# Optimization experiments

Measured on AMD Instinct MI355X. Metric: run time of the kernel, lower is better.

Reference implementation:

```python
import jax, jax.numpy as jnp
import numpy as np

N_NODES = 100000
N_EDGES = 1600000
N_GRAPHS = 256
D_IN = 128
D_HID = 128
D_OUT = 7
BN_EPS = 1e-5


def setup_inputs() -> dict:
    key = jax.random.key(0)
    ks = jax.random.split(key, 16)
    def lin(k, fan_in, fan_out):
        # torch.nn.Linear init: U(-1/sqrt(fan_in), 1/sqrt(fan_in)); stored as [in, out]
        bound = 1.0 / np.sqrt(fan_in)
        kw, kb = jax.random.split(k)
        w = jax.random.uniform(kw, (fan_in, fan_out), jnp.float32, -bound, bound)
        b = jax.random.uniform(kb, (fan_out,), jnp.float32, -bound, bound)
        return w, b
    x = jax.random.normal(ks[0], (N_NODES, D_IN), jnp.float32)
    edge_index = jax.random.randint(ks[1], (2, N_EDGES), 0, N_NODES, jnp.int64)
    batch = jnp.sort(jax.random.randint(ks[2], (N_NODES,), 0, N_GRAPHS, jnp.int64))
    w1a, b1a = lin(ks[3], D_IN, D_HID)
    w1b, b1b = lin(ks[4], D_HID, D_HID)
    w2a, b2a = lin(ks[5], D_HID, D_HID)
    w2b, b2b = lin(ks[6], D_HID, D_HID)
    wl, bl = lin(ks[7], D_HID, D_OUT)
    g1 = jnp.ones((D_HID,), jnp.float32); be1 = jnp.zeros((D_HID,), jnp.float32)
    g2 = jnp.ones((D_HID,), jnp.float32); be2 = jnp.zeros((D_HID,), jnp.float32)
    return {"x": x, "w1a": w1a, "b1a": b1a, "w1b": w1b, "b1b": b1b,
            "g1": g1, "be1": be1,
            "w2a": w2a, "b2a": b2a, "w2b": w2b, "b2b": b2b,
            "g2": g2, "be2": be2,
            "wl": wl, "bl": bl,
            "edge_index": edge_index, "batch": batch}


def gin_conv(x, edge_index, wa, ba, wb, bb):
    src, dst = edge_index[0], edge_index[1]
    # sum aggregation of source features at target nodes (eps = 0)
    agg = jax.ops.segment_sum(x[src], dst, num_segments=N_NODES)
    h = x + agg
    h = jnp.maximum(h @ wa + ba, 0.0)
    return h @ wb + bb


def batch_norm(x, gamma, beta):
    mean = jnp.mean(x, axis=0)
    var = jnp.mean(jnp.square(x - mean), axis=0)  # biased, training-mode stats
    return (x - mean) * (gamma / jnp.sqrt(var + BN_EPS)) + beta


def reference(x, w1a, b1a, w1b, b1b, g1, be1,
              w2a, b2a, w2b, b2b, g2, be2,
              wl, bl, edge_index, batch):
    h = gin_conv(x, edge_index, w1a, b1a, w1b, b1b)
    h = jnp.maximum(batch_norm(h, g1, be1), 0.0)
    h = gin_conv(h, edge_index, w2a, b2a, w2b, b2b)
    h = jnp.maximum(batch_norm(h, g2, be2), 0.0)
    # global mean pool over graphs
    sums = jax.ops.segment_sum(h, batch, num_segments=N_GRAPHS)
    cnts = jax.ops.segment_sum(jnp.ones((h.shape[0],), h.dtype), batch, num_segments=N_GRAPHS)
    pooled = sums / jnp.maximum(cnts, 1.0)[:, None]  # [G, D_HID]
    logits = pooled @ wl + bl
    return jax.nn.log_softmax(logits, axis=1)
```

## Files before the change

kernel.cpp:

```cpp
#include <hip/hip_runtime.h>
#include <math.h>

#define NN 100000
#define NE 1600000
#define NG 256
#define D 128
#define EPS 1e-5f
#define MAXDEG 64
#define NBINS 196
#define BINSZ 512
#define BINCAP 12288
#define GRID_BIN 250
#define EPB_A 6400
#define GRID_CAST 6250
#define GRID_TW 32
#define GRID_GEMM 782

typedef __attribute__((ext_vector_type(8))) short s16x8;
typedef __attribute__((ext_vector_type(4))) float f32x4;

__device__ __forceinline__ ushort f2b(float f) {
    uint u = __float_as_uint(f);
    uint r = (u + 0x7fffu + ((u >> 16) & 1u)) >> 16;
    return (ushort)r;
}
__device__ __forceinline__ float blo(uint u) { return __uint_as_float(u << 16); }
__device__ __forceinline__ float bhi(uint u) { return __uint_as_float(u & 0xFFFF0000u); }

#define SWZW(lin) ((lin) ^ ((((lin) >> 8) & 7) << 4))

__global__ __launch_bounds__(256) void prep1(const int* __restrict__ esrc, const int* __restrict__ edst,
                                             uint* __restrict__ binbuf, int* __restrict__ bincnt,
                                             const float* __restrict__ x, ushort* __restrict__ xb,
                                             const float* __restrict__ w1a, const float* __restrict__ w1b,
                                             const float* __restrict__ w2a, const float* __restrict__ w2b,
                                             ushort* __restrict__ Wt) {
    int b = blockIdx.x;
    if (b < GRID_BIN) {
        __shared__ int cnt[NBINS], lbase[NBINS];
        const int ebase = b * EPB_A;
        for (int it = 0; it < 7; ++it) {
            for (int t = threadIdx.x; t < NBINS; t += 256) cnt[t] = 0;
            __syncthreads();
            int e = ebase + it * 1024 + threadIdx.x * 4;
            bool valid = (e < ebase + EPB_A);
            int4 s = make_int4(0, 0, 0, 0), d = make_int4(0, 0, 0, 0);
            if (valid) {
                s = *(const int4*)(esrc + e);
                d = *(const int4*)(edst + e);
            }
            int b0 = d.x >> 9, b1 = d.y >> 9, b2 = d.z >> 9, b3 = d.w >> 9;
            int o0 = 0, o1 = 0, o2 = 0, o3 = 0;
            if (valid) {
                o0 = atomicAdd(&cnt[b0], 1);
                o1 = atomicAdd(&cnt[b1], 1);
                o2 = atomicAdd(&cnt[b2], 1);
                o3 = atomicAdd(&cnt[b3], 1);
            }
            __syncthreads();
            for (int t = threadIdx.x; t < NBINS; t += 256)
                lbase[t] = (cnt[t] > 0) ? atomicAdd(&bincnt[t], cnt[t]) : 0;
            __syncthreads();
            if (valid) {
                uint p0 = (uint)(lbase[b0] + o0), p1 = (uint)(lbase[b1] + o1);
                uint p2 = (uint)(lbase[b2] + o2), p3 = (uint)(lbase[b3] + o3);
                if (p0 < BINCAP) binbuf[b0 * BINCAP + p0] = ((uint)(d.x & 511) << 17) | (uint)s.x;
                if (p1 < BINCAP) binbuf[b1 * BINCAP + p1] = ((uint)(d.y & 511) << 17) | (uint)s.y;
                if (p2 < BINCAP) binbuf[b2 * BINCAP + p2] = ((uint)(d.z & 511) << 17) | (uint)s.z;
                if (p3 < BINCAP) binbuf[b3 * BINCAP + p3] = ((uint)(d.w & 511) << 17) | (uint)s.w;
            }
        }
    } else if (b < GRID_BIN + GRID_CAST) {
        int i = (b - GRID_BIN) * 256 + threadIdx.x;
        if (i * 8 < NN * D) {
            float4 v0 = *(const float4*)(x + i * 8);
            float4 v1 = *(const float4*)(x + i * 8 + 4);
            ushort o[8] = {f2b(v0.x), f2b(v0.y), f2b(v0.z), f2b(v0.w),
                           f2b(v1.x), f2b(v1.y), f2b(v1.z), f2b(v1.w)};
            *(uint4*)(xb + i * 8) = *(uint4*)o;
        }
    } else {
        int by = b - GRID_BIN - GRID_CAST;
        int wsel = by >> 3, bx = by & 7;
        const float* W = (wsel == 0) ? w1a : (wsel == 1) ? w1b : (wsel == 2) ? w2a : w2b;
        ushort* T = Wt + wsel * 16384;
        for (int i = bx * 256 + threadIdx.x; i < 16384; i += 8 * 256) {
            int k = i >> 7, cc = i & 127;
            T[(cc << 7) | k] = f2b(W[i]);
        }
    }
}

__global__ __launch_bounds__(256) void drain(const uint* __restrict__ binbuf, const int* __restrict__ bincnt,
                                             int* __restrict__ deg, int* __restrict__ slots) {
    const int bin = blockIdx.x;
    int n = bincnt[bin]; if (n > BINCAP) n = BINCAP;
    __shared__ int cur[BINSZ];
    cur[threadIdx.x] = 0;
    cur[threadIdx.x + 256] = 0;
    __syncthreads();
    const uint* bp = binbuf + bin * BINCAP;
    const int base = bin << 9;
    int i = threadIdx.x;
    for (; i + 768 < n; i += 1024) {
        uint u0 = bp[i], u1 = bp[i + 256], u2 = bp[i + 512], u3 = bp[i + 768];
        int l0 = u0 >> 17, l1 = u1 >> 17, l2 = u2 >> 17, l3 = u3 >> 17;
        int p0 = atomicAdd(&cur[l0], 1);
        int p1 = atomicAdd(&cur[l1], 1);
        int p2 = atomicAdd(&cur[l2], 1);
        int p3 = atomicAdd(&cur[l3], 1);
        slots[((base + l0) << 6) | (p0 & 63)] = (int)(u0 & 0x1FFFFu);
        slots[((base + l1) << 6) | (p1 & 63)] = (int)(u1 & 0x1FFFFu);
        slots[((base + l2) << 6) | (p2 & 63)] = (int)(u2 & 0x1FFFFu);
        slots[((base + l3) << 6) | (p3 & 63)] = (int)(u3 & 0x1FFFFu);
    }
    for (; i < n; i += 256) {
        uint u0 = bp[i];
        int l0 = u0 >> 17;
        int p0 = atomicAdd(&cur[l0], 1);
        slots[((base + l0) << 6) | (p0 & 63)] = (int)(u0 & 0x1FFFFu);
    }
    __syncthreads();
    int node = base + threadIdx.x;
    if (node < NN) deg[node] = cur[threadIdx.x];
    node += 256;
    if (node < NN) deg[node] = cur[threadIdx.x + 256];
}

template <int FUSE_BN>
__global__ __launch_bounds__(256) void gather_slots(ushort* __restrict__ out, const ushort* __restrict__ feat,
                                                    const int* __restrict__ deg, const int* __restrict__ slots,
                                                    const float* __restrict__ scale, const float* __restrict__ shift) {
    int node = __builtin_amdgcn_readfirstlane(blockIdx.x * 4 + (threadIdx.x >> 6));
    if (node >= NN) return;
    int lane = threadIdx.x & 63;
    int n = deg[node];
    n = (n > MAXDEG) ? MAXDEG : n;
    const int* sl = slots + (node << 6);
    float scx = 1.f, scy = 1.f, shx = 0.f, shy = 0.f;
    if (FUSE_BN) {
        float2 sc = *(const float2*)(scale + lane * 2);
        float2 sh = *(const float2*)(shift + lane * 2);
        scx = sc.x; scy = sc.y; shx = sh.x; shy = sh.y;
    }
    uint ub = *(const uint*)(feat + node * D + lane * 2);
    float axv[8], ayv[8];
#pragma unroll
    for (int j = 0; j < 8; ++j) { axv[j] = 0.f; ayv[j] = 0.f; }
    if (FUSE_BN) {
        axv[0] = fmaxf(fmaf(blo(ub), scx, shx), 0.f);
        ayv[0] = fmaxf(fmaf(bhi(ub), scy, shy), 0.f);
    } else {
        axv[0] = blo(ub); ayv[0] = bhi(ub);
    }
    int e = 0;
    for (; e + 15 < n; e += 16) {
        uint u[16];
#pragma unroll
        for (int j = 0; j < 16; ++j) u[j] = *(const uint*)(feat + sl[e + j] * D + lane * 2);
#pragma unroll
        for (int j = 0; j < 16; ++j) {
            int j8 = j & 7;
            if (FUSE_BN) {
                axv[j8] += fmaxf(fmaf(blo(u[j]), scx, shx), 0.f);
                ayv[j8] += fmaxf(fmaf(bhi(u[j]), scy, shy), 0.f);
            } else {
                axv[j8] += blo(u[j]); ayv[j8] += bhi(u[j]);
            }
        }
    }
    for (; e + 7 < n; e += 8) {
        uint u[8];
#pragma unroll
        for (int j = 0; j < 8; ++j) u[j] = *(const uint*)(feat + sl[e + j] * D + lane * 2);
#pragma unroll
        for (int j = 0; j < 8; ++j) {
            if (FUSE_BN) {
                axv[j] += fmaxf(fmaf(blo(u[j]), scx, shx), 0.f);
                ayv[j] += fmaxf(fmaf(bhi(u[j]), scy, shy), 0.f);
            } else {
                axv[j] += blo(u[j]); ayv[j] += bhi(u[j]);
            }
        }
    }
    for (; e + 3 < n; e += 4) {
        uint u[4];
#pragma unroll
        for (int j = 0; j < 4; ++j) u[j] = *(const uint*)(feat + sl[e + j] * D + lane * 2);
#pragma unroll
        for (int j = 0; j < 4; ++j) {
            if (FUSE_BN) {
                axv[j] += fmaxf(fmaf(blo(u[j]), scx, shx), 0.f);
                ayv[j] += fmaxf(fmaf(bhi(u[j]), scy, shy), 0.f);
            } else {
                axv[j] += blo(u[j]); ayv[j] += bhi(u[j]);
            }
        }
    }
    for (; e < n; ++e) {
        uint u0 = *(const uint*)(feat + sl[e] * D + lane * 2);
        if (FUSE_BN) {
            axv[0] += fmaxf(fmaf(blo(u0), scx, shx), 0.f);
            ayv[0] += fmaxf(fmaf(bhi(u0), scy, shy), 0.f);
        } else {
            axv[0] += blo(u0); ayv[0] += bhi(u0);
        }
    }
    float ax = ((axv[0] + axv[1]) + (axv[2] + axv[3])) + ((axv[4] + axv[5]) + (axv[6] + axv[7]));
    float ay = ((ayv[0] + ayv[1]) + (ayv[2] + ayv[3])) + ((ayv[4] + ayv[5]) + (ayv[6] + ayv[7]));
    uint o = (uint)f2b(ax) | ((uint)f2b(ay) << 16);
    *(uint*)(out + node * D + lane * 2) = o;
}

__global__ __launch_bounds__(512, 4) void gemm_dual(const ushort* __restrict__ G,
                                                    const ushort* __restrict__ Wta, const float* __restrict__ ba,
                                                    const ushort* __restrict__ Wtb, const float* __restrict__ bb,
                                                    ushort* __restrict__ H, float4* __restrict__ stat, int nrows) {
    __shared__ ushort wbuf[16384];
    __shared__ ushort tbuf[16384];
    __shared__ float4 red[8][64];
    char* wb = (char*)wbuf;
    char* tb = (char*)tbuf;

    const int tid = threadIdx.x;
    const int lane = tid & 63;
    const int wave = tid >> 6;
    const int lr = lane & 15;
    const int kg = lane >> 4;
    const int rloc = wave * 16 + lr;
    const int grow = blockIdx.x * 128 + rloc;
    const int growc = (grow > nrows - 1) ? (nrows - 1) : grow;
    const int wrow = lr * 256;
    const int wswz = (lr & 7) << 4;

    const ushort* gp = G + growc * D + kg * 8;
    s16x8 af0 = *(const s16x8*)(gp);
    s16x8 af1 = *(const s16x8*)(gp + 32);
    s16x8 af2 = *(const s16x8*)(gp + 64);
    s16x8 af3 = *(const s16x8*)(gp + 96);

#pragma unroll
    for (int i = 0; i < 4; ++i) {
        int lin = i * 8192 + tid * 16;
        uint4 v = *(const uint4*)((const char*)Wta + lin);
        *(uint4*)(wb + SWZW(lin)) = v;
    }
    __syncthreads();

    f32x4 acc[8];
#pragma unroll
    for (int ct = 0; ct < 8; ++ct) acc[ct] = (f32x4)0.f;

#pragma unroll
    for (int ks = 0; ks < 4; ++ks) {
        s16x8 af = (ks == 0) ? af0 : (ks == 1) ? af1 : (ks == 2) ? af2 : af3;
        const int wofs = (kg * 16 + ks * 64) ^ wswz;
#pragma unroll
        for (int ct = 0; ct < 8; ++ct) {
            s16x8 a = *(const s16x8*)(wb + wrow + ct * 4096 + wofs);
            acc[ct] = __builtin_amdgcn_mfma_f32_16x16x32_bf16(a, af, acc[ct], 0, 0, 0);
        }
    }

#pragma unroll
    for (int ct = 0; ct < 8; ++ct) {
        int k0 = ct * 16 + kg * 4;
        float4 bv = *(const float4*)(ba + k0);
        float o0 = fmaxf(acc[ct][0] + bv.x, 0.f);
        float o1 = fmaxf(acc[ct][1] + bv.y, 0.f);
        float o2 = fmaxf(acc[ct][2] + bv.z, 0.f);
        float o3 = fmaxf(acc[ct][3] + bv.w, 0.f);
        ushort pk[4] = {f2b(o0), f2b(o1), f2b(o2), f2b(o3)};
        int kb = k0 >> 3;
        int off = ((k0 >> 5) << 13) | ((kb & 3) << 11) | ((rloc ^ (kb & 7)) << 4) | ((k0 & 7) << 1);
        *(uint2*)(tb + off) = *(const uint2*)pk;
    }
    __syncthreads();

#pragma unroll
    for (int i = 0; i < 4; ++i) {
        int lin = i * 8192 + tid * 16;
        uint4 v = *(const uint4*)((const char*)Wtb + lin);
        *(uint4*)(wb + SWZW(lin)) = v;
    }
    s16x8 bf[4];
#pragma unroll
    for (int ks = 0; ks < 4; ++ks) {
        int kb = ks * 4 + kg;
        bf[ks] = *(const s16x8*)(tb + ((ks << 13) | (kg << 11) | ((rloc ^ (kb & 7)) << 4)));
    }
    __syncthreads();

#pragma unroll
    for (int ct = 0; ct < 8; ++ct) acc[ct] = (f32x4)0.f;
#pragma unroll
    for (int ks = 0; ks < 4; ++ks) {
        const int wofs = (kg * 16 + ks * 64) ^ wswz;
#pragma unroll
        for (int ct = 0; ct < 8; ++ct) {
            s16x8 a = *(const s16x8*)(wb + wrow + ct * 4096 + wofs);
            acc[ct] = __builtin_amdgcn_mfma_f32_16x16x32_bf16(a, bf[ks], acc[ct], 0, 0, 0);
        }
    }

#pragma unroll
    for (int ct = 0; ct < 8; ++ct) {
        int k0 = ct * 16 + kg * 4;
        float4 bv = *(const float4*)(bb + k0);
        uint2 pk2 = make_uint2(0u, 0u);
        if (grow < nrows) {
            float o0 = acc[ct][0] + bv.x;
            float o1 = acc[ct][1] + bv.y;
            float o2 = acc[ct][2] + bv.z;
            float o3 = acc[ct][3] + bv.w;
            ushort pk[4] = {f2b(o0), f2b(o1), f2b(o2), f2b(o3)};
            pk2 = *(const uint2*)pk;
            *(uint2*)(H + grow * D + k0) = pk2;
        }
        int kb = k0 >> 3;
        int off = ((k0 >> 5) << 13) | ((kb & 3) << 11) | ((rloc ^ (kb & 7)) << 4) | ((k0 & 7) << 1);
        *(uint2*)(tb + off) = pk2;
    }
    __syncthreads();

    {
        int c2 = tid & 63;
        int rg = tid >> 6;
        int k = c2 * 2;
        int kb = k >> 3;
        int base = ((k >> 5) << 13) | ((kb & 3) << 11) | ((k & 7) << 1);
        float s0 = 0.f, q0 = 0.f, s1 = 0.f, q1 = 0.f;
#pragma unroll 4
        for (int i = 0; i < 16; ++i) {
            int row = rg * 16 + i;
            uint u = *(const uint*)(tb + base + ((row ^ (kb & 7)) << 4));
            float lo = blo(u), hi = bhi(u);
            s0 += lo; q0 += lo * lo; s1 += hi; q1 += hi * hi;
        }
        red[rg][c2] = make_float4(s0, q0, s1, q1);
    }
    __syncthreads();
    if (tid < 64) {
        float4 r0 = red[0][tid], r1 = red[1][tid], r2 = red[2][tid], r3 = red[3][tid];
        float4 r4 = red[4][tid], r5 = red[5][tid], r6 = red[6][tid], r7 = red[7][tid];
        float4 o;
        o.x = ((r0.x + r1.x) + (r2.x + r3.x)) + ((r4.x + r5.x) + (r6.x + r7.x));
        o.y = ((r0.y + r1.y) + (r2.y + r3.y)) + ((r4.y + r5.y) + (r6.y + r7.y));
        o.z = ((r0.z + r1.z) + (r2.z + r3.z)) + ((r4.z + r5.z) + (r6.z + r7.z));
        o.w = ((r0.w + r1.w) + (r2.w + r3.w)) + ((r4.w + r5.w) + (r6.w + r7.w));
        stat[blockIdx.x * 64 + tid] = o;
    }
}

__global__ __launch_bounds__(256) void bn_reduce(const float4* __restrict__ stat, int nblk,
                                                 const float* __restrict__ gamma, const float* __restrict__ beta,
                                                 float* __restrict__ scale, float* __restrict__ shift, int nrows) {
    const int f4 = blockIdx.x;
    const int t = threadIdx.x;
    float s0 = 0.f, q0 = 0.f, s1 = 0.f, q1 = 0.f;
    for (int b = t; b < nblk; b += 256) {
        float4 v = stat[b * 64 + f4];
        s0 += v.x; q0 += v.y; s1 += v.z; q1 += v.w;
    }
    __shared__ float4 red[256];
    red[t] = make_float4(s0, q0, s1, q1);
    __syncthreads();
    for (int off = 128; off >= 1; off >>= 1) {
        if (t < off) {
            float4 a = red[t], b = red[t + off];
            red[t] = make_float4(a.x + b.x, a.y + b.y, a.z + b.z, a.w + b.w);
        }
        __syncthreads();
    }
    if (t == 0) {
        float4 v = red[0];
        int f0 = 2 * f4, f1 = 2 * f4 + 1;
        double m0 = (double)v.x / nrows, var0 = (double)v.y / nrows - m0 * m0;
        double m1 = (double)v.z / nrows, var1 = (double)v.w / nrows - m1 * m1;
        float sc0 = gamma[f0] * rsqrtf((float)var0 + EPS);
        float sc1 = gamma[f1] * rsqrtf((float)var1 + EPS);
        scale[f0] = sc0; shift[f0] = beta[f0] - (float)m0 * sc0;
        scale[f1] = sc1; shift[f1] = beta[f1] - (float)m1 * sc1;
    }
}

__global__ __launch_bounds__(256) void pool_partial(const ushort* __restrict__ h, const int* __restrict__ batch,
                                                    const float* __restrict__ scale, const float* __restrict__ shift,
                                                    float* __restrict__ pooled) {
    int wave = threadIdx.x >> 6;
    int lane = threadIdx.x & 63;
    int r0 = blockIdx.x * 64 + wave * 16;
    if (r0 >= NN) return;
    int f2 = lane * 2;
    float2 sc = *(const float2*)(scale + f2);
    float2 sh = *(const float2*)(shift + f2);
    float ax = 0.f, ay = 0.f;
    int cur = -1;
    int rend = r0 + 16; if (rend > NN) rend = NN;
    for (int r = r0; r < rend; ++r) {
        int g = batch[r];
        if (g != cur) {
            if (cur >= 0) {
                atomicAdd(&pooled[cur * D + f2], ax);
                atomicAdd(&pooled[cur * D + f2 + 1], ay);
            }
            cur = g; ax = 0.f; ay = 0.f;
        }
        uint u = *(const uint*)(h + r * D + f2);
        ax += fmaxf(fmaf(blo(u), sc.x, sh.x), 0.f);
        ay += fmaxf(fmaf(bhi(u), sc.y, sh.y), 0.f);
    }
    if (cur >= 0) {
        atomicAdd(&pooled[cur * D + f2], ax);
        atomicAdd(&pooled[cur * D + f2 + 1], ay);
    }
}

__device__ __forceinline__ int lower_bound_i(const int* a, int n, int v) {
    int lo = 0, hi = n;
    while (lo < hi) {
        int m = (lo + hi) >> 1;
        if (a[m] < v) lo = m + 1; else hi = m;
    }
    return lo;
}

__global__ __launch_bounds__(256) void head(const float* __restrict__ pooled, const int* __restrict__ batch,
                                            const float* __restrict__ wl, const float* __restrict__ bl,
                                            float* __restrict__ out) {
    int g = blockIdx.x * 256 + threadIdx.x;
    if (g >= NG) return;
    int lo = lower_bound_i(batch, NN, g);
    int hi = lower_bound_i(batch, NN, g + 1);
    float inv = 1.f / fmaxf((float)(hi - lo), 1.f);
    float logits[7];
#pragma unroll
    for (int c = 0; c < 7; ++c) logits[c] = bl[c];
    for (int k = 0; k < D; ++k) {
        float p = pooled[g * D + k] * inv;
#pragma unroll
        for (int c = 0; c < 7; ++c) logits[c] = fmaf(p, wl[k * 7 + c], logits[c]);
    }
    float m = logits[0];
#pragma unroll
    for (int c = 1; c < 7; ++c) m = fmaxf(m, logits[c]);
    float s = 0.f;
#pragma unroll
    for (int c = 0; c < 7; ++c) s += expf(logits[c] - m);
    float lse = m + logf(s);
#pragma unroll
    for (int c = 0; c < 7; ++c) out[g * 7 + c] = logits[c] - lse;
}

extern "C" void kernel_launch(void* const* d_in, const int* in_sizes, int n_in,
                              void* d_out, int out_size, void* d_ws, size_t ws_size,
                              hipStream_t stream) {
    const float* x   = (const float*)d_in[0];
    const float* w1a = (const float*)d_in[1];
    const float* b1a = (const float*)d_in[2];
    const float* w1b = (const float*)d_in[3];
    const float* b1b = (const float*)d_in[4];
    const float* g1  = (const float*)d_in[5];
    const float* be1 = (const float*)d_in[6];
    const float* w2a = (const float*)d_in[7];
    const float* b2a = (const float*)d_in[8];
    const float* w2b = (const float*)d_in[9];
    const float* b2b = (const float*)d_in[10];
    const float* g2  = (const float*)d_in[11];
    const float* be2 = (const float*)d_in[12];
    const float* wl  = (const float*)d_in[13];
    const float* bl  = (const float*)d_in[14];
    const int* ei    = (const int*)d_in[15];
    const int* batch = (const int*)d_in[16];
    float* out = (float*)d_out;

    const int* esrc = ei;
    const int* edst = ei + NE;

    char* ws = (char*)d_ws;
    ushort* B0 = (ushort*)(ws);
    ushort* B1 = (ushort*)(ws + 25600000);
    ushort* B2 = (ushort*)(ws + 51200000);
    uint* binbuf = (uint*)(ws + 25600000);
    int* slots   = (int*)(ws + 76800000);
    int* deg     = (int*)(ws + 102400000);
    int* bincnt  = (int*)(ws + 102800000);
    float* pooled = (float*)(ws + 102801024);
    float* scale1 = (float*)(ws + 102932096);
    float* shift1 = scale1 + 128;
    float* scale2 = shift1 + 128;
    float* shift2 = scale2 + 128;
    ushort* Wt    = (ushort*)(ws + 102934144);
    float4* stat  = (float4*)(ws + 103065216);
    ushort* Wt1a = Wt, *Wt1b = Wt + 16384, *Wt2a = Wt + 32768, *Wt2b = Wt + 49152;

    const int grid_prep = GRID_BIN + GRID_CAST + GRID_TW;
    const int grid_pool = (NN + 63) / 64;
    const int grid_gath = (NN + 3) / 4;

    hipMemsetAsync(bincnt, 0, 132096, stream);

    prep1<<<grid_prep, 256, 0, stream>>>(esrc, edst, binbuf, bincnt, x, B0, w1a, w1b, w2a, w2b, Wt);
    drain<<<NBINS, 256, 0, stream>>>(binbuf, bincnt, deg, slots);

    gather_slots<0><<<grid_gath, 256, 0, stream>>>(B1, B0, deg, slots, nullptr, nullptr);
    gemm_dual<<<GRID_GEMM, 512, 0, stream>>>(B1, Wt1a, b1a, Wt1b, b1b, B2, stat, NN);
    bn_reduce<<<64, 256, 0, stream>>>(stat, GRID_GEMM, g1, be1, scale1, shift1, NN);

    gather_slots<1><<<grid_gath, 256, 0, stream>>>(B0, B2, deg, slots, scale1, shift1);
    gemm_dual<<<GRID_GEMM, 512, 0, stream>>>(B0, Wt2a, b2a, Wt2b, b2b, B1, stat, NN);
    bn_reduce<<<64, 256, 0, stream>>>(stat, GRID_GEMM, g2, be2, scale2, shift2, NN);

    pool_partial<<<grid_pool, 256, 0, stream>>>(B1, batch, scale2, shift2, pooled);
    head<<<1, 256, 0, stream>>>(pooled, batch, wl, bl, out);
}
```

Measured before the change: 273.0 us.

## Fuse neighbor gather into dual-GEMM kernel via LDS staging

```diff
diff --git a/kernel.cpp b/kernel.cpp
--- a/kernel.cpp
+++ b/kernel.cpp
@@ -28,6 +28,7 @@
 __device__ __forceinline__ float bhi(uint u) { return __uint_as_float(u & 0xFFFF0000u); }
 
 #define SWZW(lin) ((lin) ^ ((((lin) >> 8) & 7) << 4))
+#define TOFF(row, k) ((((k) >> 5) << 13) | ((((k) >> 3) & 3) << 11) | ((((row) ^ (((k) >> 3) & 7))) << 4) | (((k) & 7) << 1))
 
 __global__ __launch_bounds__(256) void prep1(const int* __restrict__ esrc, const int* __restrict__ edst,
                                              uint* __restrict__ binbuf, int* __restrict__ bincnt,
@@ -128,91 +129,9 @@
 }
 
 template <int FUSE_BN>
-__global__ __launch_bounds__(256) void gather_slots(ushort* __restrict__ out, const ushort* __restrict__ feat,
+__global__ __launch_bounds__(512, 4) void gcn_layer(const ushort* __restrict__ feat,
                                                     const int* __restrict__ deg, const int* __restrict__ slots,
-                                                    const float* __restrict__ scale, const float* __restrict__ shift) {
-    int node = __builtin_amdgcn_readfirstlane(blockIdx.x * 4 + (threadIdx.x >> 6));
-    if (node >= NN) return;
-    int lane = threadIdx.x & 63;
-    int n = deg[node];
-    n = (n > MAXDEG) ? MAXDEG : n;
-    const int* sl = slots + (node << 6);
-    float scx = 1.f, scy = 1.f, shx = 0.f, shy = 0.f;
-    if (FUSE_BN) {
-        float2 sc = *(const float2*)(scale + lane * 2);
-        float2 sh = *(const float2*)(shift + lane * 2);
-        scx = sc.x; scy = sc.y; shx = sh.x; shy = sh.y;
-    }
-    uint ub = *(const uint*)(feat + node * D + lane * 2);
-    float axv[8], ayv[8];
-#pragma unroll
-    for (int j = 0; j < 8; ++j) { axv[j] = 0.f; ayv[j] = 0.f; }
-    if (FUSE_BN) {
-        axv[0] = fmaxf(fmaf(blo(ub), scx, shx), 0.f);
-        ayv[0] = fmaxf(fmaf(bhi(ub), scy, shy), 0.f);
-    } else {
-        axv[0] = blo(ub); ayv[0] = bhi(ub);
-    }
-    int e = 0;
-    for (; e + 15 < n; e += 16) {
-        uint u[16];
-#pragma unroll
-        for (int j = 0; j < 16; ++j) u[j] = *(const uint*)(feat + sl[e + j] * D + lane * 2);
-#pragma unroll
-        for (int j = 0; j < 16; ++j) {
-            int j8 = j & 7;
-            if (FUSE_BN) {
-                axv[j8] += fmaxf(fmaf(blo(u[j]), scx, shx), 0.f);
-                ayv[j8] += fmaxf(fmaf(bhi(u[j]), scy, shy), 0.f);
-            } else {
-                axv[j8] += blo(u[j]); ayv[j8] += bhi(u[j]);
-            }
-        }
-    }
-    for (; e + 7 < n; e += 8) {
-        uint u[8];
-#pragma unroll
-        for (int j = 0; j < 8; ++j) u[j] = *(const uint*)(feat + sl[e + j] * D + lane * 2);
-#pragma unroll
-        for (int j = 0; j < 8; ++j) {
-            if (FUSE_BN) {
-                axv[j] += fmaxf(fmaf(blo(u[j]), scx, shx), 0.f);
-                ayv[j] += fmaxf(fmaf(bhi(u[j]), scy, shy), 0.f);
-            } else {
-                axv[j] += blo(u[j]); ayv[j] += bhi(u[j]);
-            }
-        }
-    }
-    for (; e + 3 < n; e += 4) {
-        uint u[4];
-#pragma unroll
-        for (int j = 0; j < 4; ++j) u[j] = *(const uint*)(feat + sl[e + j] * D + lane * 2);
-#pragma unroll
-        for (int j = 0; j < 4; ++j) {
-            if (FUSE_BN) {
-                axv[j] += fmaxf(fmaf(blo(u[j]), scx, shx), 0.f);
-                ayv[j] += fmaxf(fmaf(bhi(u[j]), scy, shy), 0.f);
-            } else {
-                axv[j] += blo(u[j]); ayv[j] += bhi(u[j]);
-            }
-        }
-    }
-    for (; e < n; ++e) {
-        uint u0 = *(const uint*)(feat + sl[e] * D + lane * 2);
-        if (FUSE_BN) {
-            axv[0] += fmaxf(fmaf(blo(u0), scx, shx), 0.f);
-            ayv[0] += fmaxf(fmaf(bhi(u0), scy, shy), 0.f);
-        } else {
-            axv[0] += blo(u0); ayv[0] += bhi(u0);
-        }
-    }
-    float ax = ((axv[0] + axv[1]) + (axv[2] + axv[3])) + ((axv[4] + axv[5]) + (axv[6] + axv[7]));
-    float ay = ((ayv[0] + ayv[1]) + (ayv[2] + ayv[3])) + ((ayv[4] + ayv[5]) + (ayv[6] + ayv[7]));
-    uint o = (uint)f2b(ax) | ((uint)f2b(ay) << 16);
-    *(uint*)(out + node * D + lane * 2) = o;
-}
-
-__global__ __launch_bounds__(512, 4) void gemm_dual(const ushort* __restrict__ G,
+                                                    const float* __restrict__ scale, const float* __restrict__ shift,
                                                     const ushort* __restrict__ Wta, const float* __restrict__ ba,
                                                     const ushort* __restrict__ Wtb, const float* __restrict__ bb,
                                                     ushort* __restrict__ H, float4* __restrict__ stat, int nrows) {
@@ -229,15 +148,9 @@
     const int kg = lane >> 4;
     const int rloc = wave * 16 + lr;
     const int grow = blockIdx.x * 128 + rloc;
-    const int growc = (grow > nrows - 1) ? (nrows - 1) : grow;
+    const int nodeBase = blockIdx.x * 128 + wave * 16;
     const int wrow = lr * 256;
     const int wswz = (lr & 7) << 4;
-
-    const ushort* gp = G + growc * D + kg * 8;
-    s16x8 af0 = *(const s16x8*)(gp);
-    s16x8 af1 = *(const s16x8*)(gp + 32);
-    s16x8 af2 = *(const s16x8*)(gp + 64);
-    s16x8 af3 = *(const s16x8*)(gp + 96);
 
 #pragma unroll
     for (int i = 0; i < 4; ++i) {
@@ -245,7 +158,102 @@
         uint4 v = *(const uint4*)((const char*)Wta + lin);
         *(uint4*)(wb + SWZW(lin)) = v;
     }
-    __syncthreads();
+
+    {
+        float scx = 1.f, scy = 1.f, shx = 0.f, shy = 0.f;
+        if (FUSE_BN) {
+            float2 sc = *(const float2*)(scale + lane * 2);
+            float2 sh = *(const float2*)(shift + lane * 2);
+            scx = sc.x; scy = sc.y; shx = sh.x; shy = sh.y;
+        }
+        const int kG = lane * 2;
+        const int kbG = kG >> 3;
+        for (int r = 0; r < 16; ++r) {
+            int node = nodeBase + r;
+            uint o = 0u;
+            if (node < nrows) {
+                int n = deg[node];
+                n = (n > MAXDEG) ? MAXDEG : n;
+                const int* sl = slots + (node << 6);
+                uint ub = *(const uint*)(feat + node * D + lane * 2);
+                float axv[8], ayv[8];
+#pragma unroll
+                for (int j = 0; j < 8; ++j) { axv[j] = 0.f; ayv[j] = 0.f; }
+                if (FUSE_BN) {
+                    axv[0] = fmaxf(fmaf(blo(ub), scx, shx), 0.f);
+                    ayv[0] = fmaxf(fmaf(bhi(ub), scy, shy), 0.f);
+                } else {
+                    axv[0] = blo(ub); ayv[0] = bhi(ub);
+                }
+                int e = 0;
+                for (; e + 15 < n; e += 16) {
+                    uint u[16];
+#pragma unroll
+                    for (int j = 0; j < 16; ++j) u[j] = *(const uint*)(feat + sl[e + j] * D + lane * 2);
+#pragma unroll
+                    for (int j = 0; j < 16; ++j) {
+                        int j8 = j & 7;
+                        if (FUSE_BN) {
+                            axv[j8] += fmaxf(fmaf(blo(u[j]), scx, shx), 0.f);
+                            ayv[j8] += fmaxf(fmaf(bhi(u[j]), scy, shy), 0.f);
+                        } else {
+                            axv[j8] += blo(u[j]); ayv[j8] += bhi(u[j]);
+                        }
+                    }
+                }
+                for (; e + 7 < n; e += 8) {
+                    uint u[8];
+#pragma unroll
+                    for (int j = 0; j < 8; ++j) u[j] = *(const uint*)(feat + sl[e + j] * D + lane * 2);
+#pragma unroll
+                    for (int j = 0; j < 8; ++j) {
+                        if (FUSE_BN) {
+                            axv[j] += fmaxf(fmaf(blo(u[j]), scx, shx), 0.f);
+                            ayv[j] += fmaxf(fmaf(bhi(u[j]), scy, shy), 0.f);
+                        } else {
+                            axv[j] += blo(u[j]); ayv[j] += bhi(u[j]);
+                        }
+                    }
+                }
+                for (; e + 3 < n; e += 4) {
+                    uint u[4];
+#pragma unroll
+                    for (int j = 0; j < 4; ++j) u[j] = *(const uint*)(feat + sl[e + j] * D + lane * 2);
+#pragma unroll
+                    for (int j = 0; j < 4; ++j) {
+                        if (FUSE_BN) {
+                            axv[j] += fmaxf(fmaf(blo(u[j]), scx, shx), 0.f);
+                            ayv[j] += fmaxf(fmaf(bhi(u[j]), scy, shy), 0.f);
+                        } else {
+                            axv[j] += blo(u[j]); ayv[j] += bhi(u[j]);
+                        }
+                    }
+                }
+                for (; e < n; ++e) {
+                    uint u0 = *(const uint*)(feat + sl[e] * D + lane * 2);
+                    if (FUSE_BN) {
+                        axv[0] += fmaxf(fmaf(blo(u0), scx, shx), 0.f);
+                        ayv[0] += fmaxf(fmaf(bhi(u0), scy, shy), 0.f);
+                    } else {
+                        axv[0] += blo(u0); ayv[0] += bhi(u0);
+                    }
+                }
+                float ax = ((axv[0] + axv[1]) + (axv[2] + axv[3])) + ((axv[4] + axv[5]) + (axv[6] + axv[7]));
+                float ay = ((ayv[0] + ayv[1]) + (ayv[2] + ayv[3])) + ((ayv[4] + ayv[5]) + (ayv[6] + ayv[7]));
+                o = (uint)f2b(ax) | ((uint)f2b(ay) << 16);
+            }
+            int row = wave * 16 + r;
+            *(uint*)(tb + TOFF(row, kG)) = o;
+        }
+    }
+    __syncthreads();
+
+    s16x8 af[4];
+#pragma unroll
+    for (int ks = 0; ks < 4; ++ks) {
+        int kb = ks * 4 + kg;
+        af[ks] = *(const s16x8*)(tb + ((ks << 13) | (kg << 11) | ((rloc ^ (kb & 7)) << 4)));
+    }
 
     f32x4 acc[8];
 #pragma unroll
@@ -253,12 +261,11 @@
 
 #pragma unroll
     for (int ks = 0; ks < 4; ++ks) {
-        s16x8 af = (ks == 0) ? af0 : (ks == 1) ? af1 : (ks == 2) ? af2 : af3;
         const int wofs = (kg * 16 + ks * 64) ^ wswz;
 #pragma unroll
         for (int ct = 0; ct < 8; ++ct) {
             s16x8 a = *(const s16x8*)(wb + wrow + ct * 4096 + wofs);
-            acc[ct] = __builtin_amdgcn_mfma_f32_16x16x32_bf16(a, af, acc[ct], 0, 0, 0);
+            acc[ct] = __builtin_amdgcn_mfma_f32_16x16x32_bf16(a, af[ks], acc[ct], 0, 0, 0);
         }
     }
 
@@ -271,9 +278,13 @@
         float o2 = fmaxf(acc[ct][2] + bv.z, 0.f);
         float o3 = fmaxf(acc[ct][3] + bv.w, 0.f);
         ushort pk[4] = {f2b(o0), f2b(o1), f2b(o2), f2b(o3)};
-        int kb = k0 >> 3;
-        int off = ((k0 >> 5) << 13) | ((kb & 3) << 11) | ((rloc ^ (kb & 7)) << 4) | ((k0 & 7) << 1);
-        *(uint2*)(tb + off) = *(const uint2*)pk;
+        *(uint2*)(tb + TOFF(rloc, k0)) = *(const uint2*)pk;
+    }
+    s16x8 bf[4];
+#pragma unroll
+    for (int ks = 0; ks < 4; ++ks) {
+        int kb = ks * 4 + kg;
+        bf[ks] = *(const s16x8*)(tb + ((ks << 13) | (kg << 11) | ((rloc ^ (kb & 7)) << 4)));
     }
     __syncthreads();
 
@@ -282,12 +293,6 @@
         int lin = i * 8192 + tid * 16;
         uint4 v = *(const uint4*)((const char*)Wtb + lin);
         *(uint4*)(wb + SWZW(lin)) = v;
-    }
-    s16x8 bf[4];
-#pragma unroll
-    for (int ks = 0; ks < 4; ++ks) {
-        int kb = ks * 4 + kg;
-        bf[ks] = *(const s16x8*)(tb + ((ks << 13) | (kg << 11) | ((rloc ^ (kb & 7)) << 4)));
     }
     __syncthreads();
 
@@ -317,9 +322,7 @@
             pk2 = *(const uint2*)pk;
             *(uint2*)(H + grow * D + k0) = pk2;
         }
-        int kb = k0 >> 3;
-        int off = ((k0 >> 5) << 13) | ((kb & 3) << 11) | ((rloc ^ (kb & 7)) << 4) | ((k0 & 7) << 1);
-        *(uint2*)(tb + off) = pk2;
+        *(uint2*)(tb + TOFF(rloc, k0)) = pk2;
     }
     __syncthreads();
 
@@ -496,19 +499,18 @@
 
     const int grid_prep = GRID_BIN + GRID_CAST + GRID_TW;
     const int grid_pool = (NN + 63) / 64;
-    const int grid_gath = (NN + 3) / 4;
 
     hipMemsetAsync(bincnt, 0, 132096, stream);
 
     prep1<<<grid_prep, 256, 0, stream>>>(esrc, edst, binbuf, bincnt, x, B0, w1a, w1b, w2a, w2b, Wt);
     drain<<<NBINS, 256, 0, stream>>>(binbuf, bincnt, deg, slots);
 
-    gather_slots<0><<<grid_gath, 256, 0, stream>>>(B1, B0, deg, slots, nullptr, nullptr);
-    gemm_dual<<<GRID_GEMM, 512, 0, stream>>>(B1, Wt1a, b1a, Wt1b, b1b, B2, stat, NN);
+    gcn_layer<0><<<GRID_GEMM, 512, 0, stream>>>(B0, deg, slots, nullptr, nullptr,
+                                                Wt1a, b1a, Wt1b, b1b, B2, stat, NN);
     bn_reduce<<<64, 256, 0, stream>>>(stat, GRID_GEMM, g1, be1, scale1, shift1, NN);
 
-    gather_slots<1><<<grid_gath, 256, 0, stream>>>(B0, B2, deg, slots, scale1, shift1);
-    gemm_dual<<<GRID_GEMM, 512, 0, stream>>>(B0, Wt2a, b2a, Wt2b, b2b, B1, stat, NN);
+    gcn_layer<1><<<GRID_GEMM, 512, 0, stream>>>(B2, deg, slots, scale1, shift1,
+                                                Wt2a, b2a, Wt2b, b2b, B1, stat, NN);
     bn_reduce<<<64, 256, 0, stream>>>(stat, GRID_GEMM, g2, be2, scale2, shift2, NN);
 
     pool_partial<<<grid_pool, 256, 0, stream>>>(B1, batch, scale2, shift2, pooled);
```

Result: slower. 339.7 us (+24.4%).
